# Performance work log

Measured on AMD Instinct MI355X. Metric: run time of the kernel, lower is better.

The kernel has to match this reference:

```python
import jax, jax.numpy as jnp
import numpy as np

B, T, H, E = 4, 4096, 12, 64
M = 266                 # nb_features = int(64 * ln 64)
SOFTMAX_EPS = 1e-4
NORM_EPS = 1e-6


def _gaussian_orthogonal_random_matrix(nrows, ncols, seed=0):
    # blockwise QR of gaussian blocks, chi-distributed row norms (scaling=0)
    rs = np.random.RandomState(seed)
    nb_full = nrows // ncols
    blocks = []
    for _ in range(nb_full):
        q, _ = np.linalg.qr(rs.randn(ncols, ncols))
        blocks.append(q.T)
    rem = nrows - nb_full * ncols
    if rem > 0:
        q, _ = np.linalg.qr(rs.randn(ncols, ncols))
        blocks.append(q.T[:rem])
    mat = np.concatenate(blocks, axis=0)
    multiplier = np.linalg.norm(rs.randn(nrows, ncols), axis=1, keepdims=True)
    return (multiplier * mat).astype(np.float32)


def setup_inputs() -> dict:
    key = jax.random.key(0)
    k1, k2, k3 = jax.random.split(key, 3)
    query = jax.random.normal(k1, (B, T, H, E), jnp.float32)
    key_t = jax.random.normal(k2, (B, T, H, E), jnp.float32)
    value = jax.random.normal(k3, (B, T, H, E), jnp.float32)
    projection_matrix = jnp.asarray(_gaussian_orthogonal_random_matrix(M, E))
    return {"query": query, "key": key_t, "value": value,
            "projection_matrix": projection_matrix}


def _softmax_kernel(data, proj, is_query):
    # data: [B,H,T,E], proj: [M,E]  -> random features [B,H,T,M]
    data_normalizer = data.shape[-1] ** -0.25          # softmax_temp=None default
    ratio = proj.shape[0] ** -0.5
    dn = data_normalizer * data
    data_dash = jnp.einsum('bhte,me->bhtm', dn, proj)
    diag = 0.5 * jnp.sum(dn * dn, axis=-1, keepdims=True)   # [B,H,T,1]
    if is_query:
        mx = jnp.max(data_dash, axis=-1, keepdims=True)
    else:
        mx = jnp.max(data_dash, axis=(-1, -2), keepdims=True)
    return ratio * (jnp.exp(data_dash - diag - mx) + SOFTMAX_EPS)


def _causal_linear_attention(q, k, v, eps):
    # q,k: [B,H,T,M]; v: [B,H,T,D]. Recurrence: S_t = S_{t-1} + k_t v_t^T.
    qT = jnp.moveaxis(q, 2, 0)   # [T,B,H,M]
    kT = jnp.moveaxis(k, 2, 0)
    vT = jnp.moveaxis(v, 2, 0)   # [T,B,H,D]
    Bq, Hq = q.shape[0], q.shape[1]
    Mf, D = q.shape[-1], v.shape[-1]
    s0 = jnp.zeros((Bq, Hq, Mf, D), q.dtype)
    z0 = jnp.zeros((Bq, Hq, Mf), q.dtype)

    def step(carry, xs):
        s, z = carry
        q_t, k_t, v_t = xs
        s = s + jnp.einsum('bhm,bhd->bhmd', k_t, v_t)
        z = z + k_t
        num = jnp.einsum('bhm,bhmd->bhd', q_t, s)
        den = jnp.einsum('bhm,bhm->bh', q_t, z) + eps
        return (s, z), num / den[..., None]

    _, outT = jax.lax.scan(step, (s0, z0), (qT, kT, vT))  # [T,B,H,D]
    return jnp.moveaxis(outT, 0, 2)                       # [B,H,T,D]


def reference(query, key, value, projection_matrix):
    # b t h e -> b h t e
    q = jnp.transpose(query, (0, 2, 1, 3))
    k = jnp.transpose(key, (0, 2, 1, 3))
    v = jnp.transpose(value, (0, 2, 1, 3))
    q = _softmax_kernel(q, projection_matrix, is_query=True)
    k = _softmax_kernel(k, projection_matrix, is_query=False)
    out = _causal_linear_attention(q, k, v, NORM_EPS)     # [B,H,T,D]
    return jnp.transpose(out, (0, 2, 1, 3))               # b s h d
```

## Files before the change

### kernel.cpp

```cpp
#include <hip/hip_runtime.h>
#include <hip/hip_bf16.h>


typedef unsigned short u16;
typedef __attribute__((ext_vector_type(8))) short bf16x8;
typedef __attribute__((ext_vector_type(4))) float f32x4;

constexpr int Tn = 4096, Hn = 12;
constexpr int MP = 288;
constexpr int Mn = 266;
constexpr int CH = 128;
constexpr int NC = 32;
constexpr int BH = 48;

constexpr float DATA_NORM = 0.35355339059327379f;
constexpr float SM_EPS = 1e-4f;
constexpr float N_EPS  = 1e-6f;
constexpr float RATIO  = 0.06131393152401153f;

__constant__ signed char qTT[36] = {0,1,2,3,4,5,6,7,1,2,3,4,5,6,7,
                                    2,3,4,5,6,7,3,4,5,6,7,
                                    4,5,6,7,5,6,7,
                                    6,7,7};
__constant__ signed char qTP[36] = {0,0,0,0,0,0,0,0,1,1,1,1,1,1,1,
                                    2,2,2,2,2,2,3,3,3,3,3,
                                    4,4,4,4,5,5,5,
                                    6,6,7};
__constant__ int qOFF[5] = {0, 15, 26, 33, 36};

__device__ __forceinline__ u16 f2bf(float f) {
  __hip_bfloat16 h = __float2bfloat16(f);
  return __builtin_bit_cast(u16, h);
}
__device__ __forceinline__ float bf2f(u16 u) {
  return __uint_as_float(((unsigned)u) << 16);
}
__device__ __forceinline__ bf16x8 ldb(const u16* p) {
  return *reinterpret_cast<const bf16x8*>(p);
}
__device__ __forceinline__ f32x4 mfma16(bf16x8 a, bf16x8 b, f32x4 c) {
  return __builtin_amdgcn_mfma_f32_16x16x32_bf16(a, b, c, 0, 0, 0);
}
__device__ __forceinline__ void atomicMaxF(float* addr, float val) {
  if (val >= 0.f) atomicMax(reinterpret_cast<int*>(addr), __float_as_int(val));
  else atomicMin(reinterpret_cast<unsigned int*>(addr), __float_as_uint(val));
}
__device__ __forceinline__ void unpack8v(uint4 r, float* f) {
  f[0] = __uint_as_float(r.x << 16);
  f[1] = __uint_as_float(r.x & 0xffff0000u);
  f[2] = __uint_as_float(r.y << 16);
  f[3] = __uint_as_float(r.y & 0xffff0000u);
  f[4] = __uint_as_float(r.z << 16);
  f[5] = __uint_as_float(r.z & 0xffff0000u);
  f[6] = __uint_as_float(r.w << 16);
  f[7] = __uint_as_float(r.w & 0xffff0000u);
}
__device__ __forceinline__ uint4 pack8(const float* f) {
  uint4 r;
  r.x = (unsigned)f2bf(f[0]) | ((unsigned)f2bf(f[1]) << 16);
  r.y = (unsigned)f2bf(f[2]) | ((unsigned)f2bf(f[3]) << 16);
  r.z = (unsigned)f2bf(f[4]) | ((unsigned)f2bf(f[5]) << 16);
  r.w = (unsigned)f2bf(f[6]) | ((unsigned)f2bf(f[7]) << 16);
  return r;
}

__global__ void prep(const float* __restrict__ proj, u16* __restrict__ projbf,
                     float* __restrict__ kmax) {
  int idx = blockIdx.x * 256 + threadIdx.x;
  if (idx < MP * 64) {
    int m = idx >> 6, e = idx & 63;
    float v = (m < Mn) ? proj[m * 64 + e] : 0.f;
    projbf[idx] = f2bf(v);
  }
  if (blockIdx.x == 0 && threadIdx.x < BH) kmax[threadIdx.x] = -3.0e38f;
}

__global__ __launch_bounds__(512, 4) void feat_q(
    const float* __restrict__ q, const u16* __restrict__ projbf,
    u16* __restrict__ phiq) {
  __shared__ __align__(16) u16 xt[128 * 72];
  __shared__ __align__(16) u16 phib[64 * 296];
  __shared__ float diag[128];
  const int tid = threadIdx.x;
  const int bh = blockIdx.x >> 5, tb = blockIdx.x & 31;
  const int b = bh / Hn, h = bh % Hn;
  const int t0 = tb * 128;
  {
    const int t = tid >> 2, e0 = (tid & 3) * 16;
    const float* row = q + (((size_t)b * Tn + t0 + t) * Hn + h) * 64 + e0;
    float ss = 0.f;
#pragma unroll
    for (int q4 = 0; q4 < 4; ++q4) {
      float4 vv = *reinterpret_cast<const float4*>(row + q4 * 4);
      float x0 = vv.x * DATA_NORM, x1 = vv.y * DATA_NORM;
      float x2 = vv.z * DATA_NORM, x3 = vv.w * DATA_NORM;
      ss += x0 * x0 + x1 * x1 + x2 * x2 + x3 * x3;
      ushort4 uu = make_ushort4(f2bf(x0), f2bf(x1), f2bf(x2), f2bf(x3));
      *reinterpret_cast<ushort4*>(&xt[t * 72 + e0 + q4 * 4]) = uu;
    }
    ss += __shfl_xor(ss, 1);
    ss += __shfl_xor(ss, 2);
    if ((tid & 3) == 0) diag[t] = 0.5f * ss;
  }
  __syncthreads();
  const int lane = tid & 63, wv = tid >> 6;
  const int lj = lane & 15, lg = lane >> 4;
  bf16x8 a0 = ldb(&xt[(wv * 16 + lj) * 72 + lg * 8]);
  bf16x8 a1 = ldb(&xt[(wv * 16 + lj) * 72 + 32 + lg * 8]);
  f32x4 acc[17];
#pragma unroll
  for (int mt = 0; mt < 17; ++mt) {
    const u16* br = &projbf[(mt * 16 + lj) * 64 + lg * 8];
    f32x4 z = {0.f, 0.f, 0.f, 0.f};
    z = mfma16(a0, ldb(br), z);
    z = mfma16(a1, ldb(br + 32), z);
    acc[mt] = z;
  }
  float rmax[4] = {-3e38f, -3e38f, -3e38f, -3e38f};
#pragma unroll
  for (int mt = 0; mt < 17; ++mt) {
    int m = mt * 16 + lj;
    if (m < Mn) {
#pragma unroll
      for (int r = 0; r < 4; ++r) rmax[r] = fmaxf(rmax[r], acc[mt][r]);
    }
  }
#pragma unroll
  for (int r = 0; r < 4; ++r) {
    rmax[r] = fmaxf(rmax[r], __shfl_xor(rmax[r], 1));
    rmax[r] = fmaxf(rmax[r], __shfl_xor(rmax[r], 2));
    rmax[r] = fmaxf(rmax[r], __shfl_xor(rmax[r], 4));
    rmax[r] = fmaxf(rmax[r], __shfl_xor(rmax[r], 8));
  }
  float dg[4];
#pragma unroll
  for (int r = 0; r < 4; ++r) dg[r] = diag[wv * 16 + lg * 4 + r];
#pragma unroll
  for (int mt = 0; mt < 17; ++mt) {
    int m = mt * 16 + lj;
#pragma unroll
    for (int r = 0; r < 4; ++r) {
      float val = 0.f;
      if (m < Mn)
        val = RATIO * (__expf(acc[mt][r] - dg[r] - rmax[r]) + SM_EPS);
      acc[mt][r] = val;
    }
  }
  const uint4 z4 = make_uint4(0, 0, 0, 0);
  for (int hf = 0; hf < 2; ++hf) {
    __syncthreads();
    if ((wv >> 2) == hf) {
#pragma unroll
      for (int mt = 0; mt < 17; ++mt) {
#pragma unroll
        for (int r = 0; r < 4; ++r)
          phib[((wv & 3) * 16 + lg * 4 + r) * 296 + mt * 16 + lj] =
              f2bf(acc[mt][r]);
      }
    }
    __syncthreads();
    u16* ob2 = phiq + ((size_t)bh * Tn + t0 + hf * 64) * MP;
#pragma unroll
    for (int l = 0; l < 5; ++l) {
      int idx = tid + l * 512;
      if (idx < 2304) {
        int row = idx / 36, c8 = (idx % 36) * 8;
        uint4 o = (c8 >= 272) ? z4
                              : *reinterpret_cast<const uint4*>(&phib[row * 296 + c8]);
        *reinterpret_cast<uint4*>(&ob2[(size_t)row * MP + c8]) = o;
      }
    }
  }
}

__global__ __launch_bounds__(512) void feat_k(
    const float* __restrict__ k, const u16* __restrict__ projbf,
    float* __restrict__ kmax) {
  __shared__ __align__(16) u16 xt[128 * 72];
  __shared__ float wred[8];
  const int tid = threadIdx.x;
  const int bh = blockIdx.x >> 5, tb = blockIdx.x & 31;
  const int b = bh / Hn, h = bh % Hn;
  const int t0 = tb * 128;
  {
    const int t = tid >> 2, e0 = (tid & 3) * 16;
    const float* row = k + (((size_t)b * Tn + t0 + t) * Hn + h) * 64 + e0;
#pragma unroll
    for (int q4 = 0; q4 < 4; ++q4) {
      float4 vv = *reinterpret_cast<const float4*>(row + q4 * 4);
      ushort4 uu = make_ushort4(f2bf(vv.x * DATA_NORM), f2bf(vv.y * DATA_NORM),
                                f2bf(vv.z * DATA_NORM), f2bf(vv.w * DATA_NORM));
      *reinterpret_cast<ushort4*>(&xt[t * 72 + e0 + q4 * 4]) = uu;
    }
  }
  __syncthreads();
  const int lane = tid & 63, wv = tid >> 6;
  const int lj = lane & 15, lg = lane >> 4;
  bf16x8 a0 = ldb(&xt[(wv * 16 + lj) * 72 + lg * 8]);
  bf16x8 a1 = ldb(&xt[(wv * 16 + lj) * 72 + 32 + lg * 8]);
  float mx = -3e38f;
#pragma unroll
  for (int mt = 0; mt < 17; ++mt) {
    const u16* br = &projbf[(mt * 16 + lj) * 64 + lg * 8];
    f32x4 z = {0.f, 0.f, 0.f, 0.f};
    z = mfma16(a0, ldb(br), z);
    z = mfma16(a1, ldb(br + 32), z);
    int m = mt * 16 + lj;
    if (m < Mn)
      mx = fmaxf(mx, fmaxf(fmaxf(z[0], z[1]), fmaxf(z[2], z[3])));
  }
  mx = fmaxf(mx, __shfl_xor(mx, 1));
  mx = fmaxf(mx, __shfl_xor(mx, 2));
  mx = fmaxf(mx, __shfl_xor(mx, 4));
  mx = fmaxf(mx, __shfl_xor(mx, 8));
  mx = fmaxf(mx, __shfl_xor(mx, 16));
  mx = fmaxf(mx, __shfl_xor(mx, 32));
  if (lane == 0) wred[wv] = mx;
  __syncthreads();
  if (tid == 0) {
    float m2 = wred[0];
#pragma unroll
    for (int i = 1; i < 8; ++i) m2 = fmaxf(m2, wred[i]);
    atomicMaxF(&kmax[bh], m2);
  }
}

__global__ __launch_bounds__(512) void stage_a(
    const float* __restrict__ v, const float* __restrict__ kk,
    const u16* __restrict__ projbf, const float* __restrict__ kmax,
    u16* __restrict__ kvT, float* __restrict__ zp) {
  __shared__ __align__(16) u16 knl[128 * 72];
  __shared__ __align__(16) u16 Vt[64 * 136];
  __shared__ __align__(16) u16 strip[288 * 40];
  __shared__ float dkl[128];
  const int tid = threadIdx.x, lane = tid & 63, wv = tid >> 6;
  const int lj = lane & 15, lg = lane >> 4;
  const int c = blockIdx.x & 31, bh = blockIdx.x >> 5;
  const int b = bh / Hn, h = bh % Hn;
  const int t0 = c * CH;
  const float kmx = kmax[bh];

#pragma unroll
  for (int l = 0; l < 2; ++l) {
    int idx = tid + l * 512;
    int t = idx >> 3, e8 = (idx & 7) * 8;
    const float* kr = &kk[(((size_t)b * Tn + t0 + t) * Hn + h) * 64 + e8];
    float4 u0 = *reinterpret_cast<const float4*>(kr);
    float4 u1 = *reinterpret_cast<const float4*>(kr + 4);
    float x0 = u0.x * DATA_NORM, x1 = u0.y * DATA_NORM;
    float x2 = u0.z * DATA_NORM, x3 = u0.w * DATA_NORM;
    float x4 = u1.x * DATA_NORM, x5 = u1.y * DATA_NORM;
    float x6 = u1.z * DATA_NORM, x7 = u1.w * DATA_NORM;
    float ss = x0*x0 + x1*x1 + x2*x2 + x3*x3 + x4*x4 + x5*x5 + x6*x6 + x7*x7;
    *reinterpret_cast<ushort4*>(&knl[t * 72 + e8]) =
        make_ushort4(f2bf(x0), f2bf(x1), f2bf(x2), f2bf(x3));
    *reinterpret_cast<ushort4*>(&knl[t * 72 + e8 + 4]) =
        make_ushort4(f2bf(x4), f2bf(x5), f2bf(x6), f2bf(x7));
    ss += __shfl_xor(ss, 1);
    ss += __shfl_xor(ss, 2);
    ss += __shfl_xor(ss, 4);
    if ((tid & 7) == 0) dkl[t] = 0.5f * ss;
  }
#pragma unroll
  for (int l = 0; l < 4; ++l) {
    int idx = tid + l * 512;
    int t = idx >> 4, d4 = (idx & 15) * 4;
    float4 vv = *reinterpret_cast<const float4*>(
        &v[(((size_t)b * Tn + t0 + t) * Hn + h) * 64 + d4]);
    Vt[(d4 + 0) * 136 + t] = f2bf(vv.x);
    Vt[(d4 + 1) * 136 + t] = f2bf(vv.y);
    Vt[(d4 + 2) * 136 + t] = f2bf(vv.z);
    Vt[(d4 + 3) * 136 + t] = f2bf(vv.w);
  }

  float zacc = 0.f;
  f32x4 kvacc[9];
#pragma unroll
  for (int i = 0; i < 9; ++i) kvacc[i] = (f32x4){0.f, 0.f, 0.f, 0.f};
  const int dtile = wv & 3, mg = wv >> 2;
  __syncthreads();

  for (int s = 0; s < 4; ++s) {
    if (s) __syncthreads();
#pragma unroll
    for (int i = 0; i < 5; ++i) {
      int idx = wv + 8 * i;
      if (idx < 36) {
        int mt = idx % 18, th = idx / 18;
        const u16* ar = &projbf[(mt * 16 + lj) * 64 + lg * 8];
        int trow = s * 32 + th * 16 + lj;
        const u16* br = &knl[trow * 72 + lg * 8];
        f32x4 z = {0.f, 0.f, 0.f, 0.f};
        z = mfma16(ldb(ar), ldb(br), z);
        z = mfma16(ldb(ar + 32), ldb(br + 32), z);
        float dgk = dkl[trow];
#pragma unroll
        for (int r = 0; r < 4; ++r) {
          int m = mt * 16 + lg * 4 + r;
          float val = (m < Mn) ? RATIO * (__expf(z[r] - dgk - kmx) + SM_EPS) : 0.f;
          strip[m * 40 + th * 16 + lj] = f2bf(val);
        }
      }
    }
    __syncthreads();
    if (tid < MP) {
      const u16* srow = &strip[tid * 40];
#pragma unroll
      for (int o = 0; o < 32; o += 8) {
        bf16x8 vv = ldb(srow + o);
#pragma unroll
        for (int e = 0; e < 8; ++e) zacc += bf2f((u16)vv[e]);
      }
    }
    {
      bf16x8 av = ldb(&Vt[(dtile * 16 + lj) * 136 + s * 32 + lg * 8]);
#pragma unroll
      for (int i = 0; i < 9; ++i) {
        int mt = mg * 9 + i;
        kvacc[i] = mfma16(av, ldb(&strip[(mt * 16 + lj) * 40 + lg * 8]), kvacc[i]);
      }
    }
  }
  if (tid < MP) zp[((size_t)bh * NC + c) * MP + tid] = zacc;

  const size_t base2 = ((size_t)(bh * NC + c) * 64) * MP;
  for (int half = 0; half < 2; ++half) {
    __syncthreads();
    if ((dtile >> 1) == half) {
#pragma unroll
      for (int i = 0; i < 9; ++i) {
        int mt = mg * 9 + i;
#pragma unroll
        for (int r = 0; r < 4; ++r)
          strip[((dtile & 1) * 16 + lg * 4 + r) * 296 + mt * 16 + lj] =
              f2bf(kvacc[i][r]);
      }
    }
    __syncthreads();
#pragma unroll
    for (int l = 0; l < 3; ++l) {
      int idx = tid + l * 512;
      if (idx < 1152) {
        int row = idx / 36, c8 = (idx % 36) * 8;
        *reinterpret_cast<uint4*>(&kvT[base2 + (size_t)(half * 32 + row) * MP + c8]) =
            *reinterpret_cast<const uint4*>(&strip[row * 296 + c8]);
      }
    }
  }
}

__global__ void scan_kv(u16* __restrict__ kvT) {
  int idx = blockIdx.x * 256 + threadIdx.x;
  if (idx >= BH * 64 * 36) return;
  int m8 = (idx % 36) * 8;
  int r = idx / 36;
  int d = r & 63, bh = r >> 6;
  u16* p = kvT + ((size_t)(bh * NC) * 64 + d) * MP + m8;
  const size_t cs = (size_t)64 * MP;
  float acc[8];
#pragma unroll
  for (int qq = 0; qq < 8; ++qq) acc[qq] = 0.f;
  for (int c = 0; c < NC; ++c) {
    uint4 raw = *reinterpret_cast<const uint4*>(p + c * cs);
    float in[8];
    unpack8v(raw, in);
    *reinterpret_cast<uint4*>(p + c * cs) = pack8(acc);
#pragma unroll
    for (int qq = 0; qq < 8; ++qq) acc[qq] += in[qq];
  }
}

__global__ void scan_z(float* __restrict__ zp) {
  int idx = blockIdx.x * 256 + threadIdx.x;
  if (idx >= BH * MP) return;
  int m = idx % MP, bh = idx / MP;
  float* p = zp + (size_t)bh * NC * MP + m;
  float acc = 0.f;
  for (int c = 0; c < NC; ++c) {
    float x = p[(size_t)c * MP];
    p[(size_t)c * MP] = acc;
    acc += x;
  }
}

__global__ __launch_bounds__(512, 4) void stage_c(
    const float* __restrict__ v, const float* __restrict__ kk,
    const u16* __restrict__ projbf, const float* __restrict__ kmax,
    const u16* __restrict__ phiq, const u16* __restrict__ kvT,
    const float* __restrict__ zp, float* __restrict__ out) {
  __shared__ __align__(16) u16 Albuf[128 * 136];
  __shared__ __align__(16) u16 arena[32 * 296 + 32 * 72];
  __shared__ float zl[MP];
  __shared__ float dklq[32];
  __shared__ float rs2[128 * 8];
  __shared__ float qzb[128];
  __shared__ float den[128];

  u16* phik_q = arena;
  u16* knq    = arena + 32 * 296;

  const int tid = threadIdx.x, lane = tid & 63, wv = tid >> 6;
  const int lj = lane & 15, lg = lane >> 4;
  const int c = blockIdx.x & 31, bh = blockIdx.x >> 5;
  const int b = bh / Hn, h = bh % Hn;
  const int t0 = c * CH;
  const float kmx = kmax[bh];
  const size_t qbase = ((size_t)bh * Tn + t0) * MP;

  if (tid < MP) zl[tid] = zp[((size_t)bh * NC + c) * MP + tid];
#pragma unroll
  for (int l = 0; l < 5; ++l) {
    int idx = tid + l * 512;
    if (idx < 2176)
      *reinterpret_cast<uint4*>(&Albuf[idx * 8]) = make_uint4(0, 0, 0, 0);
  }
  for (int idx = tid; idx < 128 * 8; idx += 512) rs2[idx] = 0.f;

  for (int qq = 0; qq < 4; ++qq) {
    const int beg = qOFF[qq], end = qOFF[qq + 1];
    const int ia = beg + wv, ib = beg + wv + 8;
    const bool ha = ia < end, hb = ib < end;
    const int tta = ha ? qTT[ia] : 0, tpa = ha ? qTP[ia] : 0;
    const int ttb = hb ? qTT[ib] : 0, tpb = hb ? qTP[ib] : 0;

    bf16x8 aA[9], aB[9];
    if (ha) {
#pragma unroll
      for (int ks = 0; ks < 9; ++ks)
        aA[ks] = ldb(&phiq[qbase + (size_t)(tta * 16 + lj) * MP + ks * 32 + lg * 8]);
    }
    if (hb) {
#pragma unroll
      for (int ks = 0; ks < 9; ++ks)
        aB[ks] = ldb(&phiq[qbase + (size_t)(ttb * 16 + lj) * MP + ks * 32 + lg * 8]);
    }
    __builtin_amdgcn_sched_barrier(0);

    if (tid < 256) {
      int t = tid >> 3, e8 = (tid & 7) * 8;
      const float* kr = &kk[(((size_t)b * Tn + t0 + qq * 32 + t) * Hn + h) * 64 + e8];
      float4 u0 = *reinterpret_cast<const float4*>(kr);
      float4 u1 = *reinterpret_cast<const float4*>(kr + 4);
      float x0 = u0.x * DATA_NORM, x1 = u0.y * DATA_NORM;
      float x2 = u0.z * DATA_NORM, x3 = u0.w * DATA_NORM;
      float x4 = u1.x * DATA_NORM, x5 = u1.y * DATA_NORM;
      float x6 = u1.z * DATA_NORM, x7 = u1.w * DATA_NORM;
      float ss = x0*x0 + x1*x1 + x2*x2 + x3*x3 + x4*x4 + x5*x5 + x6*x6 + x7*x7;
      *reinterpret_cast<ushort4*>(&knq[t * 72 + e8]) =
          make_ushort4(f2bf(x0), f2bf(x1), f2bf(x2), f2bf(x3));
      *reinterpret_cast<ushort4*>(&knq[t * 72 + e8 + 4]) =
          make_ushort4(f2bf(x4), f2bf(x5), f2bf(x6), f2bf(x7));
      ss += __shfl_xor(ss, 1);
      ss += __shfl_xor(ss, 2);
      ss += __shfl_xor(ss, 4);
      if ((tid & 7) == 0) dklq[t] = 0.5f * ss;
    }
    __syncthreads();

    for (int u = wv; u < 36; u += 8) {
      int t2 = u / 18, mt = u % 18;
      bf16x8 a0 = ldb(&knq[(t2 * 16 + lj) * 72 + lg * 8]);
      bf16x8 a1 = ldb(&knq[(t2 * 16 + lj) * 72 + 32 + lg * 8]);
      const u16* br = &projbf[(mt * 16 + lj) * 64 + lg * 8];
      f32x4 z = {0.f, 0.f, 0.f, 0.f};
      z = mfma16(a0, ldb(br), z);
      z = mfma16(a1, ldb(br + 32), z);
      int m = mt * 16 + lj;
      int tq = t2 * 16 + lg * 4;
#pragma unroll
      for (int r = 0; r < 4; ++r) {
        float val = (m < Mn)
            ? RATIO * (__expf(z[r] - dklq[tq + r] - kmx) + SM_EPS) : 0.f;
        phik_q[(tq + r) * 296 + m] = f2bf(val);
      }
    }
    __syncthreads();

    f32x4 accA = {0.f, 0.f, 0.f, 0.f}, accB = {0.f, 0.f, 0.f, 0.f};
    if (ha) {
      __builtin_amdgcn_s_setprio(1);
#pragma unroll
      for (int ks = 0; ks < 9; ++ks) {
        int m0 = ks * 32;
        accA = mfma16(aA[ks],
                      ldb(&phik_q[((tpa & 1) * 16 + lj) * 296 + m0 + lg * 8]), accA);
        if (hb)
          accB = mfma16(aB[ks],
                        ldb(&phik_q[((tpb & 1) * 16 + lj) * 296 + m0 + lg * 8]), accB);
      }
      __builtin_amdgcn_s_setprio(0);
#pragma unroll
      for (int pick = 0; pick < 2; ++pick) {
        if (pick == 1 && !hb) break;
        int tt = pick ? ttb : tta, tp = pick ? tpb : tpa;
        f32x4 a = pick ? accB : accA;
        if (tt == tp) {
#pragma unroll
          for (int r = 0; r < 4; ++r)
            if (lj > lg * 4 + r) a[r] = 0.f;
        }
        f32x4 s = a;
#pragma unroll
        for (int r = 0; r < 4; ++r) {
          s[r] += __shfl_xor(s[r], 1);
          s[r] += __shfl_xor(s[r], 2);
          s[r] += __shfl_xor(s[r], 4);
          s[r] += __shfl_xor(s[r], 8);
        }
        if (lj == 0) {
#pragma unroll
          for (int r = 0; r < 4; ++r) rs2[(tt * 16 + lg * 4 + r) * 8 + tp] = s[r];
        }
#pragma unroll
        for (int r = 0; r < 4; ++r)
          Albuf[(tt * 16 + lg * 4 + r) * 136 + tp * 16 + lj] = f2bf(a[r]);
      }
    }
    __syncthreads();
  }

  u16* Vt = arena;
#pragma unroll
  for (int l = 0; l < 4; ++l) {
    int idx = tid + l * 512;
    int t = idx >> 4, d4 = (idx & 15) * 4;
    float4 vv = *reinterpret_cast<const float4*>(
        &v[(((size_t)b * Tn + t0 + t) * Hn + h) * 64 + d4]);
    Vt[(d4 + 0) * 136 + t] = f2bf(vv.x);
    Vt[(d4 + 1) * 136 + t] = f2bf(vv.y);
    Vt[(d4 + 2) * 136 + t] = f2bf(vv.z);
    Vt[(d4 + 3) * 136 + t] = f2bf(vv.w);
  }

  const size_t kvbase = ((size_t)(bh * NC + c) * 64) * MP;
  bf16x8 qa[9];
#pragma unroll
  for (int ks = 0; ks < 9; ++ks)
    qa[ks] = ldb(&phiq[qbase + (size_t)(wv * 16 + lj) * MP + ks * 32 + lg * 8]);
  bf16x8 kbA[4], kbB[4];
#pragma unroll
  for (int dt = 0; dt < 4; ++dt)
    kbA[dt] = ldb(&kvT[kvbase + (size_t)(dt * 16 + lj) * MP + lg * 8]);
  __builtin_amdgcn_sched_barrier(0);
  __syncthreads();

  f32x4 oacc[4];
#pragma unroll
  for (int dt = 0; dt < 4; ++dt) oacc[dt] = (f32x4){0.f, 0.f, 0.f, 0.f};
  const int ksteps = (wv >> 1) + 1;
  __builtin_amdgcn_s_setprio(1);
  for (int ks = 0; ks < ksteps; ++ks) {
    bf16x8 af = ldb(&Albuf[(wv * 16 + lj) * 136 + ks * 32 + lg * 8]);
#pragma unroll
    for (int dt = 0; dt < 4; ++dt) {
      bf16x8 bf = ldb(&Vt[(dt * 16 + lj) * 136 + ks * 32 + lg * 8]);
      oacc[dt] = mfma16(af, bf, oacc[dt]);
    }
  }
  __builtin_amdgcn_s_setprio(0);

  float qz = 0.f;
#pragma unroll
  for (int ks = 0; ks < 9; ++ks) {
    const bf16x8* cur = (ks & 1) ? kbB : kbA;
    bf16x8* nxt = (ks & 1) ? kbA : kbB;
    if (ks < 8) {
      int m1 = (ks + 1) * 32;
#pragma unroll
      for (int dt = 0; dt < 4; ++dt)
        nxt[dt] = ldb(&kvT[kvbase + (size_t)(dt * 16 + lj) * MP + m1 + lg * 8]);
    }
#pragma unroll
    for (int e = 0; e < 8; ++e)
      qz += bf2f((u16)qa[ks][e]) * zl[ks * 32 + lg * 8 + e];
#pragma unroll
    for (int dt = 0; dt < 4; ++dt)
      oacc[dt] = mfma16(qa[ks], cur[dt], oacc[dt]);
  }
  qz += __shfl_xor(qz, 16);
  qz += __shfl_xor(qz, 32);
  if (lane < 16) qzb[wv * 16 + lane] = qz;
  __syncthreads();

  if (tid < 128) {
    float s = qzb[tid] + N_EPS;
#pragma unroll
    for (int t2 = 0; t2 < 8; ++t2) s += rs2[tid * 8 + t2];
    den[tid] = s;
  }
  __syncthreads();

#pragma unroll
  for (int dt = 0; dt < 4; ++dt) {
#pragma unroll
    for (int r = 0; r < 4; ++r) {
      int tl = wv * 16 + lg * 4 + r;
      float o = oacc[dt][r] / den[tl];
      out[(((size_t)b * Tn + t0 + tl) * Hn + h) * 64 + dt * 16 + lj] = o;
    }
  }
}

extern "C" void kernel_launch(void* const* d_in, const int* in_sizes, int n_in,
                              void* d_out, int out_size, void* d_ws, size_t ws_size,
                              hipStream_t stream) {
  const float* q = (const float*)d_in[0];
  const float* k = (const float*)d_in[1];
  const float* v = (const float*)d_in[2];
  const float* proj = (const float*)d_in[3];
  float* out = (float*)d_out;

  char* ws = (char*)d_ws;
  const size_t phiq_b = (size_t)BH * Tn * MP * 2;
  const size_t kvT_b  = (size_t)BH * NC * 64 * MP * 2;
  const size_t zp_b   = (size_t)BH * NC * MP * 4;
  const size_t pj_b   = (size_t)MP * 64 * 2;

  size_t off = 0;
  u16*   phiq  = (u16*)(ws + off);  off += phiq_b;
  u16*   kvT   = (u16*)(ws + off);  off += kvT_b;
  float* zp    = (float*)(ws + off); off += zp_b;
  u16*   projbf= (u16*)(ws + off);  off += pj_b;
  float* kmax  = (float*)(ws + off);

  prep<<<72, 256, 0, stream>>>(proj, projbf, kmax);
  feat_k<<<BH * 32, 512, 0, stream>>>(k, projbf, kmax);
  feat_q<<<BH * 32, 512, 0, stream>>>(q, projbf, phiq);
  stage_a<<<BH * NC, 512, 0, stream>>>(v, k, projbf, kmax, kvT, zp);
  scan_kv<<<(BH * 64 * 36 + 255) / 256, 256, 0, stream>>>(kvT);
  scan_z<<<(BH * MP + 255) / 256, 256, 0, stream>>>(zp);
  stage_c<<<BH * NC, 512, 0, stream>>>(v, k, projbf, kmax, phiq, kvT, zp, out);
}
```

Measured before the change: 371.5 us.

## Assign intra-chunk tiles per wave, reuse q fragments, pack lower-triangular score buffer

Stage_c now assigns each wave its own query row tile (wave wv handles key tiles 0..wv), so the q feature fragments loaded once into registers are reused for both the intra-chunk scores and the inter-chunk kvT product. The per-step lookup tables and duplicate phiq loads go away. The score buffer is stored packed as a lower triangle, which removes the zero-fill, and the row sums are now computed from the bf16 buffer instead of through shuffle reductions. V is transposed into its own LDS region at kernel start so the load overlaps with other work. The cost is uneven work across waves and row sums taken from bf16-rounded values, which changes precision slightly.

```diff
diff --git a/kernel.cpp b/kernel.cpp
--- a/kernel.cpp
+++ b/kernel.cpp
@@ -17,16 +17,6 @@
 constexpr float SM_EPS = 1e-4f;
 constexpr float N_EPS  = 1e-6f;
 constexpr float RATIO  = 0.06131393152401153f;
-
-__constant__ signed char qTT[36] = {0,1,2,3,4,5,6,7,1,2,3,4,5,6,7,
-                                    2,3,4,5,6,7,3,4,5,6,7,
-                                    4,5,6,7,5,6,7,
-                                    6,7,7};
-__constant__ signed char qTP[36] = {0,0,0,0,0,0,0,0,1,1,1,1,1,1,1,
-                                    2,2,2,2,2,2,3,3,3,3,3,
-                                    4,4,4,4,5,5,5,
-                                    6,6,7};
-__constant__ int qOFF[5] = {0, 15, 26, 33, 36};
 
 __device__ __forceinline__ u16 f2bf(float f) {
   __hip_bfloat16 h = __float2bfloat16(f);
@@ -388,16 +378,14 @@
     const u16* __restrict__ projbf, const float* __restrict__ kmax,
     const u16* __restrict__ phiq, const u16* __restrict__ kvT,
     const float* __restrict__ zp, float* __restrict__ out) {
-  __shared__ __align__(16) u16 Albuf[128 * 136];
-  __shared__ __align__(16) u16 arena[32 * 296 + 32 * 72];
+  __shared__ __align__(16) u16 Albuf[9216];
+  __shared__ __align__(16) u16 phik_q[32 * 296];
+  __shared__ __align__(16) u16 knq[32 * 72];
+  __shared__ __align__(16) u16 Vt[64 * 136];
   __shared__ float zl[MP];
   __shared__ float dklq[32];
-  __shared__ float rs2[128 * 8];
   __shared__ float qzb[128];
   __shared__ float den[128];
-
-  u16* phik_q = arena;
-  u16* knq    = arena + 32 * 296;
 
   const int tid = threadIdx.x, lane = tid & 63, wv = tid >> 6;
   const int lj = lane & 15, lg = lane >> 4;
@@ -406,36 +394,28 @@
   const int t0 = c * CH;
   const float kmx = kmax[bh];
   const size_t qbase = ((size_t)bh * Tn + t0) * MP;
+  const size_t kvbase = ((size_t)(bh * NC + c) * 64) * MP;
+
+  bf16x8 qa[9];
+#pragma unroll
+  for (int ks = 0; ks < 9; ++ks)
+    qa[ks] = ldb(&phiq[qbase + (size_t)(wv * 16 + lj) * MP + ks * 32 + lg * 8]);
+  __builtin_amdgcn_sched_barrier(0);
 
   if (tid < MP) zl[tid] = zp[((size_t)bh * NC + c) * MP + tid];
 #pragma unroll
-  for (int l = 0; l < 5; ++l) {
+  for (int l = 0; l < 4; ++l) {
     int idx = tid + l * 512;
-    if (idx < 2176)
-      *reinterpret_cast<uint4*>(&Albuf[idx * 8]) = make_uint4(0, 0, 0, 0);
-  }
-  for (int idx = tid; idx < 128 * 8; idx += 512) rs2[idx] = 0.f;
+    int t = idx >> 4, d4 = (idx & 15) * 4;
+    float4 vv = *reinterpret_cast<const float4*>(
+        &v[(((size_t)b * Tn + t0 + t) * Hn + h) * 64 + d4]);
+    Vt[(d4 + 0) * 136 + t] = f2bf(vv.x);
+    Vt[(d4 + 1) * 136 + t] = f2bf(vv.y);
+    Vt[(d4 + 2) * 136 + t] = f2bf(vv.z);
+    Vt[(d4 + 3) * 136 + t] = f2bf(vv.w);
+  }
 
   for (int qq = 0; qq < 4; ++qq) {
-    const int beg = qOFF[qq], end = qOFF[qq + 1];
-    const int ia = beg + wv, ib = beg + wv + 8;
-    const bool ha = ia < end, hb = ib < end;
-    const int tta = ha ? qTT[ia] : 0, tpa = ha ? qTP[ia] : 0;
-    const int ttb = hb ? qTT[ib] : 0, tpb = hb ? qTP[ib] : 0;
-
-    bf16x8 aA[9], aB[9];
-    if (ha) {
-#pragma unroll
-      for (int ks = 0; ks < 9; ++ks)
-        aA[ks] = ldb(&phiq[qbase + (size_t)(tta * 16 + lj) * MP + ks * 32 + lg * 8]);
-    }
-    if (hb) {
-#pragma unroll
-      for (int ks = 0; ks < 9; ++ks)
-        aB[ks] = ldb(&phiq[qbase + (size_t)(ttb * 16 + lj) * MP + ks * 32 + lg * 8]);
-    }
-    __builtin_amdgcn_sched_barrier(0);
-
     if (tid < 256) {
       int t = tid >> 3, e8 = (tid & 7) * 8;
       const float* kr = &kk[(((size_t)b * Tn + t0 + qq * 32 + t) * Hn + h) * 64 + e8];
@@ -476,81 +456,55 @@
     }
     __syncthreads();
 
-    f32x4 accA = {0.f, 0.f, 0.f, 0.f}, accB = {0.f, 0.f, 0.f, 0.f};
+    const int tp0 = 2 * qq, tp1 = 2 * qq + 1;
+    const bool ha = (tp0 <= wv), hb = (tp1 <= wv);
     if (ha) {
+      f32x4 accA = {0.f, 0.f, 0.f, 0.f}, accB = {0.f, 0.f, 0.f, 0.f};
       __builtin_amdgcn_s_setprio(1);
 #pragma unroll
       for (int ks = 0; ks < 9; ++ks) {
         int m0 = ks * 32;
-        accA = mfma16(aA[ks],
-                      ldb(&phik_q[((tpa & 1) * 16 + lj) * 296 + m0 + lg * 8]), accA);
+        accA = mfma16(qa[ks], ldb(&phik_q[lj * 296 + m0 + lg * 8]), accA);
         if (hb)
-          accB = mfma16(aB[ks],
-                        ldb(&phik_q[((tpb & 1) * 16 + lj) * 296 + m0 + lg * 8]), accB);
+          accB = mfma16(qa[ks], ldb(&phik_q[(16 + lj) * 296 + m0 + lg * 8]), accB);
       }
       __builtin_amdgcn_s_setprio(0);
+      const int rb = 128 * wv * (wv + 1);
+      const int pitch = 16 * (wv + 1);
 #pragma unroll
       for (int pick = 0; pick < 2; ++pick) {
         if (pick == 1 && !hb) break;
-        int tt = pick ? ttb : tta, tp = pick ? tpb : tpa;
+        int tp = pick ? tp1 : tp0;
         f32x4 a = pick ? accB : accA;
-        if (tt == tp) {
+        if (tp == wv) {
 #pragma unroll
           for (int r = 0; r < 4; ++r)
             if (lj > lg * 4 + r) a[r] = 0.f;
         }
-        f32x4 s = a;
-#pragma unroll
-        for (int r = 0; r < 4; ++r) {
-          s[r] += __shfl_xor(s[r], 1);
-          s[r] += __shfl_xor(s[r], 2);
-          s[r] += __shfl_xor(s[r], 4);
-          s[r] += __shfl_xor(s[r], 8);
-        }
-        if (lj == 0) {
-#pragma unroll
-          for (int r = 0; r < 4; ++r) rs2[(tt * 16 + lg * 4 + r) * 8 + tp] = s[r];
-        }
 #pragma unroll
         for (int r = 0; r < 4; ++r)
-          Albuf[(tt * 16 + lg * 4 + r) * 136 + tp * 16 + lj] = f2bf(a[r]);
-      }
-    }
-    __syncthreads();
-  }
-
-  u16* Vt = arena;
-#pragma unroll
-  for (int l = 0; l < 4; ++l) {
-    int idx = tid + l * 512;
-    int t = idx >> 4, d4 = (idx & 15) * 4;
-    float4 vv = *reinterpret_cast<const float4*>(
-        &v[(((size_t)b * Tn + t0 + t) * Hn + h) * 64 + d4]);
-    Vt[(d4 + 0) * 136 + t] = f2bf(vv.x);
-    Vt[(d4 + 1) * 136 + t] = f2bf(vv.y);
-    Vt[(d4 + 2) * 136 + t] = f2bf(vv.z);
-    Vt[(d4 + 3) * 136 + t] = f2bf(vv.w);
-  }
-
-  const size_t kvbase = ((size_t)(bh * NC + c) * 64) * MP;
-  bf16x8 qa[9];
-#pragma unroll
-  for (int ks = 0; ks < 9; ++ks)
-    qa[ks] = ldb(&phiq[qbase + (size_t)(wv * 16 + lj) * MP + ks * 32 + lg * 8]);
+          Albuf[rb + (lg * 4 + r) * pitch + tp * 16 + lj] = f2bf(a[r]);
+      }
+    }
+    __syncthreads();
+  }
+
   bf16x8 kbA[4], kbB[4];
 #pragma unroll
   for (int dt = 0; dt < 4; ++dt)
     kbA[dt] = ldb(&kvT[kvbase + (size_t)(dt * 16 + lj) * MP + lg * 8]);
   __builtin_amdgcn_sched_barrier(0);
-  __syncthreads();
 
   f32x4 oacc[4];
 #pragma unroll
   for (int dt = 0; dt < 4; ++dt) oacc[dt] = (f32x4){0.f, 0.f, 0.f, 0.f};
   const int ksteps = (wv >> 1) + 1;
+  const int rowA = 128 * wv * (wv + 1) + lj * 16 * (wv + 1);
+  const bf16x8 zf = {0, 0, 0, 0, 0, 0, 0, 0};
   __builtin_amdgcn_s_setprio(1);
   for (int ks = 0; ks < ksteps; ++ks) {
-    bf16x8 af = ldb(&Albuf[(wv * 16 + lj) * 136 + ks * 32 + lg * 8]);
+    bool dead = ((wv & 1) == 0) && (ks == ksteps - 1) && (lg >= 2);
+    bf16x8 af = dead ? zf : ldb(&Albuf[rowA + ks * 32 + lg * 8]);
 #pragma unroll
     for (int dt = 0; dt < 4; ++dt) {
       bf16x8 bf = ldb(&Vt[(dt * 16 + lj) * 136 + ks * 32 + lg * 8]);
@@ -583,9 +537,15 @@
   __syncthreads();
 
   if (tid < 128) {
+    int tb2 = tid >> 4;
+    int Lr = 16 * (tb2 + 1);
+    const u16* arow = &Albuf[128 * tb2 * (tb2 + 1) + (tid & 15) * Lr];
     float s = qzb[tid] + N_EPS;
-#pragma unroll
-    for (int t2 = 0; t2 < 8; ++t2) s += rs2[tid * 8 + t2];
+    for (int cc = 0; cc < Lr; cc += 8) {
+      bf16x8 vv = ldb(arow + cc);
+#pragma unroll
+      for (int e = 0; e < 8; ++e) s += bf2f((u16)vv[e]);
+    }
     den[tid] = s;
   }
   __syncthreads();
```

Result: faster. 338.8 us (-8.8%).
